# Kernel optimization log

Measured on AMD Instinct MI355X. Metric: run time of the kernel, lower is better.

The kernel has to match this reference:

```python
import jax, jax.numpy as jnp
import numpy as np


def setup_inputs() -> dict:
    key = jax.random.key(0)
    ks = jax.random.split(key, 7)
    B, C, L, A = 8, 1024, 2048, 128
    x = jax.random.normal(ks[0], (B, C, L), dtype=jnp.float32)
    Wk = jax.random.normal(ks[1], (A, C), dtype=jnp.float32) * (1.0 / np.sqrt(C))
    bk = jax.random.normal(ks[2], (A,), dtype=jnp.float32) * 0.01
    Wq = jax.random.normal(ks[3], (A, C), dtype=jnp.float32) * (1.0 / np.sqrt(C))
    bq = jax.random.normal(ks[4], (A,), dtype=jnp.float32) * 0.01
    Wp = jax.random.normal(ks[5], (C, C), dtype=jnp.float32) * (1.0 / np.sqrt(C))
    bp = jax.random.normal(ks[6], (C,), dtype=jnp.float32) * 0.01
    return {"x": x, "Wk": Wk, "bk": bk, "Wq": Wq, "bq": bq, "Wp": Wp, "bp": bp}


def reference(x, Wk, bk, Wq, bq, Wp, bp):
    # x: [B, C, L]; 1x1 Conv1d == pointwise linear over channel dim
    keys = jnp.einsum('bcl,ac->bal', x, Wk) + bk[None, :, None]      # [B, A, L]
    queries = jnp.einsum('bcl,ac->bal', x, Wq) + bq[None, :, None]   # [B, A, L]
    values = jnp.einsum('bal,bam->blm', keys, queries)               # keys^T @ queries -> [B, L, L]
    seqlen = x.shape[2]
    # NOTE: source uses seqlen ** 1 / 2 which is seqlen/2 due to Python precedence
    attn = jax.nn.softmax(values / (seqlen / 2.0), axis=-1)          # [B, L, L]
    out = jnp.einsum('bcl,blm->bcm', x, attn)                        # x @ attn -> [B, C, L]
    out = jnp.einsum('bcm,dc->bdm', out, Wp) + bp[None, :, None]     # output projection
    return out
```

## Files before the change

### kernel.cpp

```cpp
#include <hip/hip_runtime.h>
#include <hip/hip_bf16.h>

typedef __hip_bfloat16 bf16;
typedef __attribute__((ext_vector_type(8))) short bfrag8;
typedef __attribute__((ext_vector_type(8))) int intx8;
typedef __attribute__((ext_vector_type(4))) float floatx4;


__device__ __forceinline__ unsigned char f2fp8(float f) {
    f = fminf(fmaxf(f, -448.f), 448.f);
    return (unsigned char)(__builtin_amdgcn_cvt_pk_fp8_f32(f, f, 0, false) & 0xFF);
}

__device__ __forceinline__ void async_copy16(const void* g, void* lds) {
    __builtin_amdgcn_global_load_lds(
        (const __attribute__((address_space(1))) unsigned int*)g,
        (__attribute__((address_space(3))) unsigned int*)lds, 16, 0, 0);
}

template<int BIASMODE, int OUTKIND, bool EXPZ, bool MFAST>
__global__ __launch_bounds__(256)
void gemm128(const bf16* __restrict__ Ag, long sAb, int lda,
             const bf16* __restrict__ Bg, long sBb, int ldb,
             void* __restrict__ Cg, long sCb, int ldc,
             const float* __restrict__ scl, const float* __restrict__ b2,
             float* __restrict__ Zp, int K, int logfast)
{
    __shared__ unsigned short As[128 * 64];
    __shared__ unsigned short Bs[128 * 64];

    const int lin = blockIdx.x;
    const int bz  = lin & 7;
    const int s   = lin >> 3;
    const int msk = (1 << logfast) - 1;
    int mT, nT;
    if (MFAST) { mT = s & msk; nT = s >> logfast; }
    else       { nT = s & msk; mT = s >> logfast; }

    const bf16* A  = Ag + (size_t)bz * sAb + (size_t)mT * 128 * lda;
    const bf16* Bp = Bg + (size_t)bz * sBb + (size_t)nT * 128 * ldb;
    const int t = threadIdx.x, wave = t >> 6, lane = t & 63;
    const int qrow = lane & 15, quad = lane >> 4;
    const int wr = (wave >> 1) * 64, wc = (wave & 1) * 64;

    floatx4 acc[4][4] = {};

    for (int k0 = 0; k0 < K; k0 += 64) {
        #pragma unroll
        for (int j = 0; j < 4; ++j) {
            int c = j * 256 + t;
            int r = c >> 3, p = c & 7;
            int g = p ^ (r & 7);
            async_copy16(A + (size_t)r * lda + k0 + g * 8, &As[c * 8]);
        }
        #pragma unroll
        for (int j = 0; j < 4; ++j) {
            int c = j * 256 + t;
            int r = c >> 3, p = c & 7;
            int g = p ^ (r & 7);
            async_copy16(Bp + (size_t)r * ldb + k0 + g * 8, &Bs[c * 8]);
        }
        __syncthreads();

        #pragma unroll
        for (int ks = 0; ks < 2; ++ks) {
            bfrag8 af[4], bfv[4];
            #pragma unroll
            for (int mi = 0; mi < 4; ++mi) {
                int row = wr + mi * 16 + qrow;
                int ck  = ks * 4 + quad;
                af[mi] = *(const bfrag8*)&As[row * 64 + ((ck ^ (row & 7)) * 8)];
            }
            #pragma unroll
            for (int ni = 0; ni < 4; ++ni) {
                int row = wc + ni * 16 + qrow;
                int ck  = ks * 4 + quad;
                bfv[ni] = *(const bfrag8*)&Bs[row * 64 + ((ck ^ (row & 7)) * 8)];
            }
            #pragma unroll
            for (int mi = 0; mi < 4; ++mi)
                #pragma unroll
                for (int ni = 0; ni < 4; ++ni)
                    acc[mi][ni] = __builtin_amdgcn_mfma_f32_16x16x32_bf16(
                        af[mi], bfv[ni], acc[mi][ni], 0, 0, 0);
        }
        __syncthreads();
    }

    const int bmr = mT * 128 + wr, bnc = nT * 128 + wc;
    float zp[4] = {0.f, 0.f, 0.f, 0.f};
    #pragma unroll
    for (int mi = 0; mi < 4; ++mi) {
        #pragma unroll
        for (int ni = 0; ni < 4; ++ni) {
            int col = bnc + ni * 16 + qrow;
            #pragma unroll
            for (int r = 0; r < 4; ++r) {
                int row = bmr + mi * 16 + quad * 4 + r;
                float v = acc[mi][ni][r];
                if (EXPZ) { float e = __expf(v); zp[ni] += e; v = (e - 1.0f) * 4096.0f; }
                if (BIASMODE == 1) v = v * scl[col] + b2[col];
                if (BIASMODE == 2) v += scl[row];
                if (OUTKIND == 1)
                    ((float*)Cg + (size_t)bz * sCb)[(size_t)row * ldc + col] = v;
                else if (OUTKIND == 0)
                    ((bf16*)Cg + (size_t)bz * sCb)[(size_t)row * ldc + col] = __float2bfloat16(v);
                else
                    ((unsigned char*)Cg + (size_t)bz * sCb)[(size_t)row * ldc + col] = f2fp8(v);
            }
        }
    }
    if (EXPZ) {
        #pragma unroll
        for (int ni = 0; ni < 4; ++ni) {
            float tt = zp[ni];
            tt += __shfl_xor(tt, 16, 64);
            tt += __shfl_xor(tt, 32, 64);
            if (quad == 0)
                atomicAdd(&Zp[bz * 2048 + bnc + ni * 16 + qrow], tt);
        }
    }
}

template<int MODE, bool MFAST>
__global__ __launch_bounds__(256)
void gemm_f8(const unsigned char* __restrict__ Ag, long sAb, int lda,
             const unsigned char* __restrict__ Bg, long sBb, int ldb,
             void* __restrict__ Cg, long sCb, int ldc,
             const float* __restrict__ rowb, float os, int K, int logfast)
{
    __shared__ unsigned char As[128 * 128];
    __shared__ unsigned char Bs[128 * 128];

    const int lin = blockIdx.x;
    const int bz  = lin & 7;
    const int s   = lin >> 3;
    const int msk = (1 << logfast) - 1;
    int mT, nT;
    if (MFAST) { mT = s & msk; nT = s >> logfast; }
    else       { nT = s & msk; mT = s >> logfast; }

    const unsigned char* A  = Ag + (size_t)bz * sAb + (size_t)mT * 128 * lda;
    const unsigned char* Bp = Bg + (size_t)bz * sBb + (size_t)nT * 128 * ldb;
    const int t = threadIdx.x, wave = t >> 6, lane = t & 63;
    const int qrow = lane & 15, quad = lane >> 4;
    const int wr = (wave >> 1) * 64, wc = (wave & 1) * 64;

    floatx4 acc[4][4] = {};

    for (int k0 = 0; k0 < K; k0 += 128) {
        #pragma unroll
        for (int j = 0; j < 4; ++j) {
            int c = j * 256 + t;
            int r = c >> 3, p = c & 7;
            int g = p ^ (r & 7);
            async_copy16(A + (size_t)r * lda + k0 + g * 16, &As[c * 16]);
        }
        #pragma unroll
        for (int j = 0; j < 4; ++j) {
            int c = j * 256 + t;
            int r = c >> 3, p = c & 7;
            int g = p ^ (r & 7);
            async_copy16(Bp + (size_t)r * ldb + k0 + g * 16, &Bs[c * 16]);
        }
        __syncthreads();

        intx8 af[4], bf[4];
        #pragma unroll
        for (int mi = 0; mi < 4; ++mi) {
            int row = wr + mi * 16 + qrow, sw = row & 7;
            union { intx8 v; uint4 q[2]; } u;
            u.q[0] = *(const uint4*)&As[row * 128 + (((quad * 2    ) ^ sw) * 16)];
            u.q[1] = *(const uint4*)&As[row * 128 + (((quad * 2 + 1) ^ sw) * 16)];
            af[mi] = u.v;
        }
        #pragma unroll
        for (int ni = 0; ni < 4; ++ni) {
            int row = wc + ni * 16 + qrow, sw = row & 7;
            union { intx8 v; uint4 q[2]; } u;
            u.q[0] = *(const uint4*)&Bs[row * 128 + (((quad * 2    ) ^ sw) * 16)];
            u.q[1] = *(const uint4*)&Bs[row * 128 + (((quad * 2 + 1) ^ sw) * 16)];
            bf[ni] = u.v;
        }
        #pragma unroll
        for (int mi = 0; mi < 4; ++mi)
            #pragma unroll
            for (int ni = 0; ni < 4; ++ni)
                acc[mi][ni] = __builtin_amdgcn_mfma_scale_f32_16x16x128_f8f6f4(
                    af[mi], bf[ni], acc[mi][ni], 0, 0, 0, 127, 0, 127);
        __syncthreads();
    }

    const int bmr = mT * 128 + wr, bnc = nT * 128 + wc;
    #pragma unroll
    for (int mi = 0; mi < 4; ++mi) {
        int row0 = bmr + mi * 16 + quad * 4;
        float4 rb4;
        if (MODE == 2) rb4 = *(const float4*)&rowb[bz * 1024 + row0];
        #pragma unroll
        for (int ni = 0; ni < 4; ++ni) {
            int col = bnc + ni * 16 + qrow;
            floatx4 a = acc[mi][ni];
            if (MODE == 2) {
                float* Co = (float*)Cg + (size_t)bz * sCb;
                Co[(size_t)(row0 + 0) * ldc + col] = a[0] * os + rb4.x;
                Co[(size_t)(row0 + 1) * ldc + col] = a[1] * os + rb4.y;
                Co[(size_t)(row0 + 2) * ldc + col] = a[2] * os + rb4.z;
                Co[(size_t)(row0 + 3) * ldc + col] = a[3] * os + rb4.w;
            } else {
                unsigned char* C8 = (unsigned char*)Cg + (size_t)bz * sCb;
                #pragma unroll
                for (int r = 0; r < 4; ++r)
                    C8[(size_t)(row0 + r) * ldc + col] = f2fp8(a[r] * os);
            }
        }
    }
}

__global__ __launch_bounds__(256)
void conv_w(const float* __restrict__ Wk, const float* __restrict__ Wq,
            const float* __restrict__ Wp, bf16* __restrict__ Wkqb,
            unsigned char* __restrict__ Wp8)
{
    int i = blockIdx.x * 256 + threadIdx.x;
    if (i < 32768) {
        const float* src = (i < 16384) ? Wk : Wq;
        int off = (i < 16384) ? i : i - 16384;
        bf16* dst = Wkqb + (size_t)((i < 16384) ? 0 : 131072);
        const float4* sp = (const float4*)src + (size_t)off * 2;
        float4 a = sp[0], b = sp[1];
        union { uint4 u; unsigned short h[8]; } o;
        union { bf16 h; unsigned short u; } cv;
        cv.h = __float2bfloat16(a.x); o.h[0] = cv.u;
        cv.h = __float2bfloat16(a.y); o.h[1] = cv.u;
        cv.h = __float2bfloat16(a.z); o.h[2] = cv.u;
        cv.h = __float2bfloat16(a.w); o.h[3] = cv.u;
        cv.h = __float2bfloat16(b.x); o.h[4] = cv.u;
        cv.h = __float2bfloat16(b.y); o.h[5] = cv.u;
        cv.h = __float2bfloat16(b.z); o.h[6] = cv.u;
        cv.h = __float2bfloat16(b.w); o.h[7] = cv.u;
        ((uint4*)dst)[off] = o.u;
    } else {
        int off = i - 32768;
        const float4* sp = (const float4*)Wp + (size_t)off * 2;
        float4 a = sp[0], b = sp[1];
        unsigned char o[8];
        o[0] = f2fp8(a.x * 2048.f); o[1] = f2fp8(a.y * 2048.f);
        o[2] = f2fp8(a.z * 2048.f); o[3] = f2fp8(a.w * 2048.f);
        o[4] = f2fp8(b.x * 2048.f); o[5] = f2fp8(b.y * 2048.f);
        o[6] = f2fp8(b.z * 2048.f); o[7] = f2fp8(b.w * 2048.f);
        uint2 w;
        w.x = (unsigned int)o[0] | ((unsigned int)o[1] << 8) | ((unsigned int)o[2] << 16) | ((unsigned int)o[3] << 24);
        w.y = (unsigned int)o[4] | ((unsigned int)o[5] << 8) | ((unsigned int)o[6] << 16) | ((unsigned int)o[7] << 24);
        ((uint2*)Wp8)[off] = w;
    }
}

__global__ __launch_bounds__(256)
void conv_x(const float* __restrict__ x, bf16* __restrict__ xt)
{
    const int b = blockIdx.z;
    const int l0 = blockIdx.x * 64, c0 = blockIdx.y * 64;
    const float* xp = x + (size_t)b * 1024 * 2048;
    bf16* xtp = xt + (size_t)b * 2048 * 1024;
    __shared__ unsigned short tile[64][65];
    const int t = threadIdx.x, tr = t >> 4, tc4 = (t & 15) * 4;
    union { bf16 h; unsigned short u; } cv;
    #pragma unroll
    for (int i = 0; i < 4; ++i) {
        int r = i * 16 + tr;
        float4 v = *(const float4*)(xp + (size_t)(c0 + r) * 2048 + l0 + tc4);
        cv.h = __float2bfloat16(v.x); tile[r][tc4]     = cv.u;
        cv.h = __float2bfloat16(v.y); tile[r][tc4 + 1] = cv.u;
        cv.h = __float2bfloat16(v.z); tile[r][tc4 + 2] = cv.u;
        cv.h = __float2bfloat16(v.w); tile[r][tc4 + 3] = cv.u;
    }
    __syncthreads();
    #pragma unroll
    for (int i = 0; i < 4; ++i) {
        int lr = i * 16 + tr;
        union { uint2 u; unsigned short h[4]; } o;
        #pragma unroll
        for (int j = 0; j < 4; ++j) o.h[j] = tile[tc4 + j][lr];
        *(uint2*)(xtp + (size_t)(l0 + lr) * 1024 + c0 + tc4) = o.u;
    }
}

__global__ void prep_bias(const float* __restrict__ bk, const float* __restrict__ bq,
                          float* __restrict__ scl, float* __restrict__ b2, float kscale)
{
    int t = threadIdx.x;
    float s = (t < 128) ? kscale : 1.0f;
    scl[t] = s;
    b2[t] = ((t < 128) ? bk[t] : bq[t - 128]) * s;
}

__global__ __launch_bounds__(256)
void normx(const float* __restrict__ x, const float* __restrict__ Z,
           unsigned char* __restrict__ xs, float* __restrict__ colsum)
{
    const int bc = blockIdx.x;
    const int b  = bc >> 10;
    const int t  = threadIdx.x;
    const float* xp = x + (size_t)bc * 2048 + t * 8;
    const float* zp = Z + b * 2048 + t * 8;
    float4 a = ((const float4*)xp)[0], c4 = ((const float4*)xp)[1];
    float4 z0 = ((const float4*)zp)[0], z1 = ((const float4*)zp)[1];
    float v[8];
    v[0] = a.x  / fmaxf(z0.x, 1e-10f); v[1] = a.y / fmaxf(z0.y, 1e-10f);
    v[2] = a.z  / fmaxf(z0.z, 1e-10f); v[3] = a.w / fmaxf(z0.w, 1e-10f);
    v[4] = c4.x / fmaxf(z1.x, 1e-10f); v[5] = c4.y / fmaxf(z1.y, 1e-10f);
    v[6] = c4.z / fmaxf(z1.z, 1e-10f); v[7] = c4.w / fmaxf(z1.w, 1e-10f);
    float s = 0.f;
    unsigned char o[8];
    #pragma unroll
    for (int j = 0; j < 8; ++j) { s += v[j]; o[j] = f2fp8(v[j] * 65536.f); }
    uint2 w;
    w.x = (unsigned int)o[0] | ((unsigned int)o[1] << 8) | ((unsigned int)o[2] << 16) | ((unsigned int)o[3] << 24);
    w.y = (unsigned int)o[4] | ((unsigned int)o[5] << 8) | ((unsigned int)o[6] << 16) | ((unsigned int)o[7] << 24);
    ((uint2*)(xs + (size_t)bc * 2048))[t] = w;
    #pragma unroll
    for (int off = 32; off >= 1; off >>= 1) s += __shfl_xor(s, off, 64);
    __shared__ float red[4];
    if ((t & 63) == 0) red[t >> 6] = s;
    __syncthreads();
    if (t == 0) colsum[bc] = red[0] + red[1] + red[2] + red[3];
}

__global__ __launch_bounds__(256)
void basek(const float* __restrict__ Wp, const float* __restrict__ colsum,
           const float* __restrict__ bp, float* __restrict__ base)
{
    const int d = blockIdx.x, t = threadIdx.x;
    float4 w = *(const float4*)(Wp + (size_t)d * 1024 + t * 4);
    float pb[8];
    #pragma unroll
    for (int b = 0; b < 8; ++b) {
        float4 cs = *(const float4*)(colsum + b * 1024 + t * 4);
        pb[b] = w.x * cs.x + w.y * cs.y + w.z * cs.z + w.w * cs.w;
    }
    __shared__ float red[8][4];
    #pragma unroll
    for (int b = 0; b < 8; ++b) {
        float s = pb[b];
        #pragma unroll
        for (int off = 32; off >= 1; off >>= 1) s += __shfl_xor(s, off, 64);
        if ((t & 63) == 0) red[b][t >> 6] = s;
    }
    __syncthreads();
    if (t < 8) base[t * 1024 + d] = bp[d] + red[t][0] + red[t][1] + red[t][2] + red[t][3];
}

extern "C" void kernel_launch(void* const* d_in, const int* in_sizes, int n_in,
                              void* d_out, int out_size, void* d_ws, size_t ws_size,
                              hipStream_t stream)
{
    const float* x  = (const float*)d_in[0];
    const float* Wk = (const float*)d_in[1];
    const float* bk = (const float*)d_in[2];
    const float* Wq = (const float*)d_in[3];
    const float* bq = (const float*)d_in[4];
    const float* Wp = (const float*)d_in[5];
    const float* bp = (const float*)d_in[6];
    float* out = (float*)d_out;

    const float kscale = 2.0f / 2048.0f;

    bf16* xt   = (bf16*)d_ws;
    bf16* KQt  = xt + (size_t)8 * 2048 * 1024;
    bf16* Wkqb = KQt + (size_t)8 * 2048 * 256;
    unsigned char* Wp8 = (unsigned char*)(Wkqb + (size_t)256 * 1024);
    unsigned char* St8 = Wp8 + (size_t)1048576;
    unsigned char* xs8 = St8 + (size_t)8 * 2048 * 2048;
    float* Z      = (float*)(xs8 + (size_t)8 * 1024 * 2048);
    float* colsum = Z + 8 * 2048;
    float* base   = colsum + 8 * 1024;
    float* scl    = base + 8 * 1024;
    float* b2     = scl + 256;
    unsigned char* Dlt = (unsigned char*)xt;

    dim3 blk(256, 1, 1);

    prep_bias<<<dim3(1), blk, 0, stream>>>(bk, bq, scl, b2, kscale);
    conv_w<<<dim3(640), blk, 0, stream>>>(Wk, Wq, Wp, Wkqb, Wp8);
    conv_x<<<dim3(32, 16, 8), blk, 0, stream>>>(x, xt);

    gemm128<1, 0, false, false><<<dim3(8 * 16 * 2), blk, 0, stream>>>(
        xt, 2048L * 1024, 1024,  Wkqb, 0, 1024,
        KQt, 2048L * 256, 256,  scl, b2, nullptr, 1024, 1);

    hipMemsetAsync(Z, 0, (size_t)8 * 2048 * sizeof(float), stream);

    gemm128<0, 2, true, false><<<dim3(8 * 16 * 16), blk, 0, stream>>>(
        KQt + 128, 2048L * 256, 256,  KQt, 2048L * 256, 256,
        St8, 2048L * 2048, 2048,  nullptr, nullptr, Z, 128, 4);

    normx<<<dim3(8 * 1024), blk, 0, stream>>>(x, Z, xs8, colsum);
    basek<<<dim3(1024), blk, 0, stream>>>(Wp, colsum, bp, base);

    gemm_f8<0, false><<<dim3(8 * 16 * 8), blk, 0, stream>>>(
        St8, 2048L * 2048, 2048,  xs8, 1024L * 2048, 2048,
        Dlt, 2048L * 1024, 1024,  nullptr, 0.0009765625f, 2048, 3);

    gemm_f8<2, true><<<dim3(8 * 8 * 16), blk, 0, stream>>>(
        Wp8, 0, 1024,  Dlt, 2048L * 1024, 1024,
        out, 1024L * 2048, 2048,  base, 1.862645149230957e-9f, 1024, 3);
}
```

Baseline: 270.7 us.

## Enlarge FP8 GEMM tiles to 256x256 with double-buffered async LDS loads

The FP8 GEMM kernel now uses 512-thread blocks computing 256x256 output tiles, with each wave holding an 8x4 accumulator grid. Global-to-LDS copies are double-buffered, with explicit vmcnt waits and barriers so the next K-tile loads while the current one feeds the MFMAs. This is meant to hide load latency and raise reuse per byte loaded. In exchange it uses 128KB of LDS and more registers, and the launch grids become smaller, which may leave some CUs idle.

```diff
diff --git a/kernel.cpp b/kernel.cpp
--- a/kernel.cpp
+++ b/kernel.cpp
@@ -123,77 +123,95 @@
 }
 
 template<int MODE, bool MFAST>
-__global__ __launch_bounds__(256)
+__global__ __launch_bounds__(512, 2)
 void gemm_f8(const unsigned char* __restrict__ Ag, long sAb, int lda,
              const unsigned char* __restrict__ Bg, long sBb, int ldb,
              void* __restrict__ Cg, long sCb, int ldc,
              const float* __restrict__ rowb, float os, int K, int logfast)
 {
-    __shared__ unsigned char As[128 * 128];
-    __shared__ unsigned char Bs[128 * 128];
+    __shared__ __align__(16) unsigned char smem[131072];
 
     const int lin = blockIdx.x;
     const int bz  = lin & 7;
-    const int s   = lin >> 3;
+    const int s0  = lin >> 3;
     const int msk = (1 << logfast) - 1;
     int mT, nT;
-    if (MFAST) { mT = s & msk; nT = s >> logfast; }
-    else       { nT = s & msk; mT = s >> logfast; }
-
-    const unsigned char* A  = Ag + (size_t)bz * sAb + (size_t)mT * 128 * lda;
-    const unsigned char* Bp = Bg + (size_t)bz * sBb + (size_t)nT * 128 * ldb;
+    if (MFAST) { mT = s0 & msk; nT = s0 >> logfast; }
+    else       { nT = s0 & msk; mT = s0 >> logfast; }
+
+    const unsigned char* A  = Ag + (size_t)bz * sAb + (size_t)mT * 256 * lda;
+    const unsigned char* Bp = Bg + (size_t)bz * sBb + (size_t)nT * 256 * ldb;
     const int t = threadIdx.x, wave = t >> 6, lane = t & 63;
     const int qrow = lane & 15, quad = lane >> 4;
-    const int wr = (wave >> 1) * 64, wc = (wave & 1) * 64;
-
-    floatx4 acc[4][4] = {};
-
-    for (int k0 = 0; k0 < K; k0 += 128) {
+    const int wm = (wave >> 2) * 128;
+    const int wn = (wave & 3) * 64;
+
+    floatx4 acc[8][4] = {};
+
+    auto stage = [&](int kt, int slot) {
+        const int k0 = kt << 7;
+        unsigned char* Ad = &smem[slot * 32768];
+        unsigned char* Bd = &smem[65536 + slot * 32768];
         #pragma unroll
         for (int j = 0; j < 4; ++j) {
-            int c = j * 256 + t;
-            int r = c >> 3, p = c & 7;
-            int g = p ^ (r & 7);
-            async_copy16(A + (size_t)r * lda + k0 + g * 16, &As[c * 16]);
+            int c = j * 512 + t;
+            int r = c >> 3, p = c & 7, g = p ^ (r & 7);
+            async_copy16(A + (size_t)r * lda + k0 + g * 16, Ad + c * 16);
         }
         #pragma unroll
         for (int j = 0; j < 4; ++j) {
-            int c = j * 256 + t;
-            int r = c >> 3, p = c & 7;
-            int g = p ^ (r & 7);
-            async_copy16(Bp + (size_t)r * ldb + k0 + g * 16, &Bs[c * 16]);
-        }
-        __syncthreads();
-
-        intx8 af[4], bf[4];
-        #pragma unroll
-        for (int mi = 0; mi < 4; ++mi) {
-            int row = wr + mi * 16 + qrow, sw = row & 7;
+            int c = j * 512 + t;
+            int r = c >> 3, p = c & 7, g = p ^ (r & 7);
+            async_copy16(Bp + (size_t)r * ldb + k0 + g * 16, Bd + c * 16);
+        }
+    };
+
+    const int NT = K >> 7;
+    stage(0, 0);
+    stage(1, 1);
+
+    for (int kt = 0; kt < NT; ++kt) {
+        const int slot = kt & 1;
+        if (kt + 1 < NT) asm volatile("s_waitcnt vmcnt(8)" ::: "memory");
+        else             asm volatile("s_waitcnt vmcnt(0)" ::: "memory");
+        __builtin_amdgcn_sched_barrier(0);
+        __builtin_amdgcn_s_barrier();
+        __builtin_amdgcn_sched_barrier(0);
+
+        const unsigned char* As = &smem[slot * 32768];
+        const unsigned char* Bs = &smem[65536 + slot * 32768];
+
+        intx8 bfr[4];
+        #pragma unroll
+        for (int ni = 0; ni < 4; ++ni) {
+            int row = wn + ni * 16 + qrow, sw = row & 7;
+            union { intx8 v; uint4 q[2]; } u;
+            u.q[0] = *(const uint4*)&Bs[row * 128 + (((quad * 2    ) ^ sw) * 16)];
+            u.q[1] = *(const uint4*)&Bs[row * 128 + (((quad * 2 + 1) ^ sw) * 16)];
+            bfr[ni] = u.v;
+        }
+        #pragma unroll
+        for (int mi = 0; mi < 8; ++mi) {
+            int row = wm + mi * 16 + qrow, sw = row & 7;
             union { intx8 v; uint4 q[2]; } u;
             u.q[0] = *(const uint4*)&As[row * 128 + (((quad * 2    ) ^ sw) * 16)];
             u.q[1] = *(const uint4*)&As[row * 128 + (((quad * 2 + 1) ^ sw) * 16)];
-            af[mi] = u.v;
-        }
-        #pragma unroll
-        for (int ni = 0; ni < 4; ++ni) {
-            int row = wc + ni * 16 + qrow, sw = row & 7;
-            union { intx8 v; uint4 q[2]; } u;
-            u.q[0] = *(const uint4*)&Bs[row * 128 + (((quad * 2    ) ^ sw) * 16)];
-            u.q[1] = *(const uint4*)&Bs[row * 128 + (((quad * 2 + 1) ^ sw) * 16)];
-            bf[ni] = u.v;
-        }
-        #pragma unroll
-        for (int mi = 0; mi < 4; ++mi)
+            intx8 af = u.v;
             #pragma unroll
             for (int ni = 0; ni < 4; ++ni)
                 acc[mi][ni] = __builtin_amdgcn_mfma_scale_f32_16x16x128_f8f6f4(
-                    af[mi], bf[ni], acc[mi][ni], 0, 0, 0, 127, 0, 127);
-        __syncthreads();
-    }
-
-    const int bmr = mT * 128 + wr, bnc = nT * 128 + wc;
-    #pragma unroll
-    for (int mi = 0; mi < 4; ++mi) {
+                    af, bfr[ni], acc[mi][ni], 0, 0, 0, 127, 0, 127);
+        }
+
+        __builtin_amdgcn_sched_barrier(0);
+        __builtin_amdgcn_s_barrier();
+        __builtin_amdgcn_sched_barrier(0);
+        if (kt + 2 < NT) stage(kt + 2, slot);
+    }
+
+    const int bmr = mT * 256 + wm, bnc = nT * 256 + wn;
+    #pragma unroll
+    for (int mi = 0; mi < 8; ++mi) {
         int row0 = bmr + mi * 16 + quad * 4;
         float4 rb4;
         if (MODE == 2) rb4 = *(const float4*)&rowb[bz * 1024 + row0];
@@ -380,6 +398,7 @@
     unsigned char* Dlt = (unsigned char*)xt;
 
     dim3 blk(256, 1, 1);
+    dim3 blk512(512, 1, 1);
 
     prep_bias<<<dim3(1), blk, 0, stream>>>(bk, bq, scl, b2, kscale);
     conv_w<<<dim3(640), blk, 0, stream>>>(Wk, Wq, Wp, Wkqb, Wp8);
@@ -398,11 +417,11 @@
     normx<<<dim3(8 * 1024), blk, 0, stream>>>(x, Z, xs8, colsum);
     basek<<<dim3(1024), blk, 0, stream>>>(Wp, colsum, bp, base);
 
-    gemm_f8<0, false><<<dim3(8 * 16 * 8), blk, 0, stream>>>(
+    gemm_f8<0, false><<<dim3(8 * 8 * 4), blk512, 0, stream>>>(
         St8, 2048L * 2048, 2048,  xs8, 1024L * 2048, 2048,
-        Dlt, 2048L * 1024, 1024,  nullptr, 0.0009765625f, 2048, 3);
-
-    gemm_f8<2, true><<<dim3(8 * 8 * 16), blk, 0, stream>>>(
+        Dlt, 2048L * 1024, 1024,  nullptr, 0.0009765625f, 2048, 2);
+
+    gemm_f8<2, true><<<dim3(8 * 4 * 8), blk512, 0, stream>>>(
         Wp8, 0, 1024,  Dlt, 2048L * 1024, 1024,
-        out, 1024L * 2048, 2048,  base, 1.862645149230957e-9f, 1024, 3);
-}
+        out, 1024L * 2048, 2048,  base, 1.862645149230957e-9f, 1024, 2);
+}
```

New measurement: 262.0 us. 3.2% less time.
